# Kernel optimization log

Measured on AMD Instinct MI355X. Metric: run time of the kernel, lower is better.

## Reference

```python
import jax, jax.numpy as jnp
import numpy as np

K = 16  # number of neighbors (self excluded), matches init k
NUM_CLASSES = 100


def setup_inputs() -> dict:
    key = jax.random.key(0)
    kx, ky = jax.random.split(key)
    N, D = 8192, 256
    x = jax.random.normal(kx, (N, D), dtype=jnp.float32)
    y = jax.random.randint(ky, (N,), 0, NUM_CLASSES, dtype=jnp.int64)
    return {"x": x, "y": y}


def _knn_loss(x, y):
    N = x.shape[0]
    k = min(K, N - 1)
    # Pairwise squared Euclidean distances via Gram trick: [N, N]
    sq_norms = jnp.sum(x * x, axis=1)
    sq = sq_norms[:, None] + sq_norms[None, :] - 2.0 * (x @ x.T)
    sq = jnp.maximum(sq, 0.0)
    eye = jnp.eye(N, dtype=bool)
    # Keep sqrt grad-safe on the (excluded) diagonal by placing a dummy 1.0 there.
    d = jnp.sqrt(jnp.where(eye, 1.0, sq))  # [N, N] Euclidean distances

    # k nearest neighbors excluding self (BallTree query k+1 then drop col 0).
    d_for_knn = jnp.where(eye, jnp.inf, d)
    _, nn_idx = jax.lax.top_k(-d_for_knn, k)  # [N, k] indices of smallest distances

    # distances = exp(-d); denominator sums over all j != i.
    exp_d = jnp.where(eye, 0.0, jnp.exp(-d))
    denom = jnp.sum(exp_d, axis=1)  # [N]

    # log(exp(-d_in) / denom_i) = -d_in - log(denom_i)
    nn_d = jnp.take_along_axis(d, nn_idx, axis=1)          # [N, k]
    log_p = -nn_d - jnp.log(denom)[:, None]                 # [N, k]

    # Only neighbors with matching label contribute; rows with none are skipped.
    match = (y[nn_idx] == y[:, None]).astype(x.dtype)       # [N, k]
    cnt = jnp.sum(match, axis=1)                            # [N]
    row_mean = jnp.where(cnt > 0, jnp.sum(log_p * match, axis=1) / jnp.maximum(cnt, 1.0), 0.0)
    return -jnp.sum(row_mean) / N


def reference(x, y):
    return _knn_loss(x, y)
```

## Files before the change

kernel.cpp:

```cpp
#include <hip/hip_runtime.h>
#include <hip/hip_fp16.h>


typedef __attribute__((ext_vector_type(8))) short s8v;
typedef __attribute__((ext_vector_type(4))) float f32x4;

#define NROW 8192
#define NK   256
#define SAMPN 512
#define TAUR  6
#define PSLOT 2

template <bool B> struct BoolC { static constexpr bool value = B; };

#define OFF_DNP  0
#define OFF_NRM  262144
#define OFF_TAU  294912
#define OFF_XB   327680
#define OFF_SAMP 4521984
#define OFF_PASS 4521984
#define PASS_BYTES (NROW * 512 * 4)

__device__ __forceinline__ unsigned short f2bf(float f) {
  unsigned u = __float_as_uint(f);
  return (unsigned short)((u + 0x7FFFu + ((u >> 16) & 1u)) >> 16);
}

__device__ __forceinline__ void gld16(const void* g, void* l) {
  __builtin_amdgcn_global_load_lds(
      (const __attribute__((address_space(1))) unsigned int*)g,
      (__attribute__((address_space(3))) unsigned int*)l, 16, 0, 0);
}

__device__ __forceinline__ unsigned umin32(unsigned a, unsigned b) { return a < b ? a : b; }

__global__ __launch_bounds__(256) void k_prep(const float* __restrict__ x,
                                              unsigned short* __restrict__ xb,
                                              float* __restrict__ nrm) {
  const int w = threadIdx.x >> 6, l = threadIdx.x & 63;
  const int r = blockIdx.x * 4 + w;
  const float4 xv = *reinterpret_cast<const float4*>(x + r * NK + l * 4);
  float ns = xv.x * xv.x + xv.y * xv.y + xv.z * xv.z + xv.w * xv.w;
  ns += __shfl_xor(ns, 1);  ns += __shfl_xor(ns, 2);  ns += __shfl_xor(ns, 4);
  ns += __shfl_xor(ns, 8);  ns += __shfl_xor(ns, 16); ns += __shfl_xor(ns, 32);
  if (l == 0) nrm[r] = ns;
  ushort4 bv;
  bv.x = f2bf(xv.x); bv.y = f2bf(xv.y); bv.z = f2bf(xv.z); bv.w = f2bf(xv.w);
  const int gs = (l >> 1) ^ (r & 7);
  *reinterpret_cast<ushort4*>(xb + r * NK + gs * 8 + (l & 1) * 4) = bv;
}

__global__ __launch_bounds__(512) void k_samp(const unsigned short* __restrict__ xb,
                                              const float* __restrict__ nrm,
                                              unsigned short* __restrict__ samp) {
  __shared__ __align__(16) unsigned short Bl[64 * NK];
  __shared__ float ncs[64];
  const int tid = threadIdx.x;
  const int w = tid >> 6, l = tid & 63, l15 = l & 15, l4 = l >> 4;
  const int rb = blockIdx.x >> 3, ss = blockIdx.x & 7;
  const int rowbase = rb * 128 + (w >> 1) * 32;
  const int wcol = (w & 1) * 32;

  #pragma unroll
  for (int jj = 0; jj < 4; ++jj) {
    const int unit = jj * 512 + tid;
    const int sc = unit >> 5, gsl = unit & 31;
    const int s = ss * 64 + sc;
    const int jrow = s * 16 + (s & 7);
    gld16(xb + jrow * NK + gsl * 8, &Bl[unit * 8]);
  }
  if (tid < 64) {
    const int s = ss * 64 + tid;
    ncs[tid] = nrm[s * 16 + (s & 7)];
  }

  s8v A[2][8];
  #pragma unroll
  for (int rf = 0; rf < 2; ++rf) {
    const int rr = rowbase + rf * 16 + l15;
    #pragma unroll
    for (int kf = 0; kf < 8; ++kf) {
      const int g = ((kf << 2) | l4) ^ (rr & 7);
      A[rf][kf] = *reinterpret_cast<const s8v*>(xb + rr * NK + g * 8);
    }
  }
  float nr[2][4];
  #pragma unroll
  for (int rf = 0; rf < 2; ++rf)
    #pragma unroll
    for (int q = 0; q < 4; ++q) nr[rf][q] = nrm[rowbase + rf * 16 + l4 * 4 + q];

  __syncthreads();
  f32x4 acc[2][2];
  #pragma unroll
  for (int rf = 0; rf < 2; ++rf) {
    f32x4 z = {0.f, 0.f, 0.f, 0.f};
    acc[rf][0] = z; acc[rf][1] = z;
  }
  #pragma unroll
  for (int kf = 0; kf < 8; ++kf) {
    const int gs = ((kf << 2) | l4) ^ (l15 & 7);
    const s8v b0 = *reinterpret_cast<const s8v*>(&Bl[(wcol + l15) * NK + gs * 8]);
    const s8v b1 = *reinterpret_cast<const s8v*>(&Bl[(wcol + 16 + l15) * NK + gs * 8]);
    #pragma unroll
    for (int rf = 0; rf < 2; ++rf) {
      acc[rf][0] = __builtin_amdgcn_mfma_f32_16x16x32_bf16(A[rf][kf], b0, acc[rf][0], 0, 0, 0);
      acc[rf][1] = __builtin_amdgcn_mfma_f32_16x16x32_bf16(A[rf][kf], b1, acc[rf][1], 0, 0, 0);
    }
  }
  #pragma unroll
  for (int rf = 0; rf < 2; ++rf)
    #pragma unroll
    for (int cf = 0; cf < 2; ++cf) {
      const int scol = ss * 64 + wcol + cf * 16 + l15;
      const int jcol = scol * 16 + (scol & 7);
      const float nc = ncs[wcol + cf * 16 + l15];
      #pragma unroll
      for (int q = 0; q < 4; ++q) {
        const int rowg = rowbase + rf * 16 + l4 * 4 + q;
        const float sq = fmaxf(fmaf(acc[rf][cf][q], -2.0f, nr[rf][q] + nc), 0.0f);
        const float dd = __builtin_amdgcn_sqrtf(sq);
        unsigned short d16 = __half_as_ushort(__float2half(dd));
        if (jcol == rowg) d16 = 0xFFFFu;
        samp[rowg * SAMPN + scol] = d16;
      }
    }
}

__global__ __launch_bounds__(256) void k_tau(const unsigned short* __restrict__ samp,
                                             unsigned* __restrict__ tauk) {
  const int w = threadIdx.x >> 6, l = threadIdx.x & 63;
  const int r = blockIdx.x * 4 + w;
  const uint4 pa = *reinterpret_cast<const uint4*>(samp + r * SAMPN + l * 8);
  unsigned v[8];
  v[0] = pa.x & 0xFFFFu; v[1] = pa.x >> 16; v[2] = pa.y & 0xFFFFu; v[3] = pa.y >> 16;
  v[4] = pa.z & 0xFFFFu; v[5] = pa.z >> 16; v[6] = pa.w & 0xFFFFu; v[7] = pa.w >> 16;
  unsigned m = 0;
  for (int pp = 0; pp < TAUR; ++pp) {
    unsigned lm = v[0];
    #pragma unroll
    for (int j = 1; j < 8; ++j) lm = umin32(lm, v[j]);
    m = lm;
    m = umin32(m, __shfl_xor(m, 1));  m = umin32(m, __shfl_xor(m, 2));
    m = umin32(m, __shfl_xor(m, 4));  m = umin32(m, __shfl_xor(m, 8));
    m = umin32(m, __shfl_xor(m, 16)); m = umin32(m, __shfl_xor(m, 32));
    const unsigned long long bal = __ballot(lm == m);
    const int owner = (int)__ffsll(bal) - 1;
    if (l == owner) {
      bool f = false;
      #pragma unroll
      for (int j = 0; j < 8; ++j)
        if (!f && v[j] == m) { v[j] = 0xFFFFFFFFu; f = true; }
    }
  }
  if (l == 0) tauk[r] = m;
}

__global__ __launch_bounds__(512) void k_main(const unsigned short* __restrict__ xb,
                                              const float* __restrict__ nrm,
                                              const unsigned* __restrict__ tauk,
                                              float* __restrict__ dnp,
                                              unsigned* __restrict__ pass) {
  __shared__ __align__(16) unsigned short Bl[2][64 * NK];
  __shared__ float ncsAll[1024];
  __shared__ float dpart[128];
  const int tid = threadIdx.x;
  const int w = tid >> 6, l = tid & 63, l15 = l & 15, l4 = l >> 4;
  const int rb = blockIdx.x >> 3, cs = blockIdx.x & 7;
  const int rowbase = rb * 128 + (w >> 1) * 32;
  const int wcol = (w & 1) * 32;
  const int colslice = cs * 1024;
  const unsigned long long ltm = (1ull << l) - 1ull;
  const unsigned long long sub = 0xFFFFull << (l4 * 16);

  if (tid < 128) dpart[tid] = 0.0f;
  ncsAll[tid]       = nrm[colslice + tid];
  ncsAll[tid + 512] = nrm[colslice + 512 + tid];

  s8v A[2][8];
  #pragma unroll
  for (int rf = 0; rf < 2; ++rf) {
    const int rr = rowbase + rf * 16 + l15;
    #pragma unroll
    for (int kf = 0; kf < 8; ++kf) {
      const int g = ((kf << 2) | l4) ^ (rr & 7);
      A[rf][kf] = *reinterpret_cast<const s8v*>(xb + rr * NK + g * 8);
    }
  }
  float nr[2][4], tk2[2][4], dn[2][4];
  #pragma unroll
  for (int rf = 0; rf < 2; ++rf)
    #pragma unroll
    for (int q = 0; q < 4; ++q) {
      const int rowg = rowbase + rf * 16 + l4 * 4 + q;
      nr[rf][q] = nrm[rowg];
      const float tw = __half2float(__ushort_as_half((unsigned short)(tauk[rowg] + 1u)));
      tk2[rf][q] = tw * tw;
      dn[rf][q] = 0.0f;
    }

  auto stage = [&](int buf, int t) {
    const unsigned short* src = xb + (colslice + t * 64) * NK;
    #pragma unroll
    for (int jj = 0; jj < 4; ++jj)
      gld16(src + (jj * 512 + tid) * 8, &Bl[buf][(jj * 512 + w * 64) * 8]);
  };

  const int tdiag = rb * 2 - cs * 16;

  stage(0, 0);
  __syncthreads();

  for (int t = 0; t < 16; ++t) {
    const int cur = t & 1;
    if (t < 15) {
      stage(cur ^ 1, t + 1);
      asm volatile("s_waitcnt vmcnt(4)" ::: "memory");
    }
    __builtin_amdgcn_s_barrier();
    __builtin_amdgcn_sched_barrier(0);
    const int cbase = colslice + t * 64;
    f32x4 acc[2][2];
    #pragma unroll
    for (int rf = 0; rf < 2; ++rf) {
      f32x4 z = {0.f, 0.f, 0.f, 0.f};
      acc[rf][0] = z; acc[rf][1] = z;
    }
    #pragma unroll
    for (int kf = 0; kf < 8; ++kf) {
      const int gs = ((kf << 2) | l4) ^ (l15 & 7);
      const s8v b0 = *reinterpret_cast<const s8v*>(&Bl[cur][(wcol + l15) * NK + gs * 8]);
      const s8v b1 = *reinterpret_cast<const s8v*>(&Bl[cur][(wcol + 16 + l15) * NK + gs * 8]);
      #pragma unroll
      for (int rf = 0; rf < 2; ++rf) {
        acc[rf][0] = __builtin_amdgcn_mfma_f32_16x16x32_bf16(A[rf][kf], b0, acc[rf][0], 0, 0, 0);
        acc[rf][1] = __builtin_amdgcn_mfma_f32_16x16x32_bf16(A[rf][kf], b1, acc[rf][1], 0, 0, 0);
      }
    }
    const float nc0 = ncsAll[t * 64 + wcol + l15];
    const float nc1 = ncsAll[t * 64 + wcol + 16 + l15];
    const int colg0 = cbase + wcol + l15;
    const int colg1 = colg0 + 16;
    const int gt4 = (cs * 16 + t) * 4;
    auto epi = [&](auto dgc) {
      constexpr bool DG = decltype(dgc)::value;
      #pragma unroll
      for (int rf = 0; rf < 2; ++rf)
        #pragma unroll
        for (int q = 0; q < 4; ++q) {
          const int rowg = rowbase + rf * 16 + l4 * 4 + q;
          float sq0 = fmaf(acc[rf][0][q], -2.0f, nr[rf][q] + nc0);
          float sq1 = fmaf(acc[rf][1][q], -2.0f, nr[rf][q] + nc1);
          if (DG) { sq0 = fmaxf(sq0, 0.0f); sq1 = fmaxf(sq1, 0.0f); }
          const float d0 = __builtin_amdgcn_sqrtf(sq0);
          const float d1 = __builtin_amdgcn_sqrtf(sq1);
          float e0 = __expf(-d0), e1 = __expf(-d1);
          bool p0 = sq0 < tk2[rf][q];
          bool p1 = sq1 < tk2[rf][q];
          if (DG) {
            const bool nd0 = (rowg != colg0), nd1 = (rowg != colg1);
            e0 = nd0 ? e0 : 0.0f;  e1 = nd1 ? e1 : 0.0f;
            p0 = p0 && nd0;  p1 = p1 && nd1;
          }
          dn[rf][q] += e0 + e1;
          const unsigned long long m0 = __ballot(p0);
          const unsigned long long m1 = __ballot(p1);
          if ((m0 | m1) != 0ull) {
            const int r0 = __popcll(m0 & sub & ltm);
            const int r1 = __popcll(m1 & sub & ltm);
            if (p0 && r0 < PSLOT) {
              const unsigned d16 = __half_as_ushort(__float2half(d0));
              pass[rowg * 512 + gt4 + r0] = (d16 << 16) | (unsigned)colg0;
            }
            if (p1 && r1 < PSLOT) {
              const unsigned d16 = __half_as_ushort(__float2half(d1));
              pass[rowg * 512 + gt4 + 2 + r1] = (d16 << 16) | (unsigned)colg1;
            }
          }
        }
    };
    if (t == tdiag || t == tdiag + 1) epi(BoolC<true>{});
    else                              epi(BoolC<false>{});
    __builtin_amdgcn_s_barrier();
  }
  #pragma unroll
  for (int rf = 0; rf < 2; ++rf)
    #pragma unroll
    for (int q = 0; q < 4; ++q) {
      float vs = dn[rf][q];
      vs += __shfl_xor(vs, 1); vs += __shfl_xor(vs, 2);
      vs += __shfl_xor(vs, 4); vs += __shfl_xor(vs, 8);
      if (l15 == 0) atomicAdd(&dpart[(w >> 1) * 32 + rf * 16 + l4 * 4 + q], vs);
    }
  __syncthreads();
  if (tid < 128) dnp[(rb * 128 + tid) * 8 + cs] = dpart[tid];
}

__global__ __launch_bounds__(256) void k_fin(const unsigned* __restrict__ pass,
                                             const float* __restrict__ dnp,
                                             const int* __restrict__ y,
                                             float* __restrict__ out) {
  const int w = threadIdx.x >> 6, l = threadIdx.x & 63;
  const int r = blockIdx.x * 4 + w;
  unsigned kk[8];
  const uint4 pa = *reinterpret_cast<const uint4*>(pass + r * 512 + l * 8);
  const uint4 pb = *reinterpret_cast<const uint4*>(pass + r * 512 + l * 8 + 4);
  kk[0] = pa.x; kk[1] = pa.y; kk[2] = pa.z; kk[3] = pa.w;
  kk[4] = pb.x; kk[5] = pb.y; kk[6] = pb.z; kk[7] = pb.w;
  unsigned myKey = 0xFFFFFFFFu;
  for (int pp = 0; pp < 16; ++pp) {
    unsigned lm = kk[0];
    #pragma unroll
    for (int j = 1; j < 8; ++j) lm = umin32(lm, kk[j]);
    unsigned m = lm;
    m = umin32(m, __shfl_xor(m, 1));  m = umin32(m, __shfl_xor(m, 2));
    m = umin32(m, __shfl_xor(m, 4));  m = umin32(m, __shfl_xor(m, 8));
    m = umin32(m, __shfl_xor(m, 16)); m = umin32(m, __shfl_xor(m, 32));
    const unsigned long long bal = __ballot(lm == m);
    const int owner = (int)__ffsll(bal) - 1;
    if (l == owner) {
      bool f = false;
      #pragma unroll
      for (int j = 0; j < 8; ++j)
        if (!f && kk[j] == m) { kk[j] = 0xFFFFFFFFu; f = true; }
    }
    if (l == pp) myKey = m;
  }
  float den = 0.0f;
  #pragma unroll
  for (int cs = 0; cs < 8; ++cs) den += dnp[r * 8 + cs];
  const float logden = __logf(den);
  float contrib = 0.0f, cmf = 0.0f;
  if (l < 16 && myKey != 0xFFFFFFFFu) {
    const int col = (int)(myKey & 0x1FFFu);
    const float dd = __half2float(__ushort_as_half((unsigned short)(myKey >> 16)));
    if (y[col] == y[r]) { contrib = -dd - logden; cmf = 1.0f; }
  }
  contrib += __shfl_xor(contrib, 1);  contrib += __shfl_xor(contrib, 2);
  contrib += __shfl_xor(contrib, 4);  contrib += __shfl_xor(contrib, 8);
  contrib += __shfl_xor(contrib, 16); contrib += __shfl_xor(contrib, 32);
  cmf += __shfl_xor(cmf, 1);  cmf += __shfl_xor(cmf, 2);
  cmf += __shfl_xor(cmf, 4);  cmf += __shfl_xor(cmf, 8);
  cmf += __shfl_xor(cmf, 16); cmf += __shfl_xor(cmf, 32);
  if (l == 0 && cmf > 0.0f)
    atomicAdd(out, (contrib / cmf) * (-1.0f / 8192.0f));
}

extern "C" void kernel_launch(void* const* d_in, const int* in_sizes, int n_in,
                              void* d_out, int out_size, void* d_ws, size_t ws_size,
                              hipStream_t stream) {
  const float* x = (const float*)d_in[0];
  const int* y = (const int*)d_in[1];
  float* out = (float*)d_out;
  char* ws = (char*)d_ws;

  float*          dnp  = (float*)(ws + OFF_DNP);
  float*          nrm  = (float*)(ws + OFF_NRM);
  unsigned*       tauk = (unsigned*)(ws + OFF_TAU);
  unsigned short* xb   = (unsigned short*)(ws + OFF_XB);
  unsigned short* samp = (unsigned short*)(ws + OFF_SAMP);
  unsigned*       pass = (unsigned*)(ws + OFF_PASS);

  k_prep<<<2048, 256, 0, stream>>>(x, xb, nrm);
  k_samp<<<512,  512, 0, stream>>>(xb, nrm, samp);
  k_tau <<<2048, 256, 0, stream>>>(samp, tauk);
  hipMemsetAsync(pass, 0xFF, PASS_BYTES, stream);
  hipMemsetAsync(d_out, 0, sizeof(float), stream);
  k_main<<<512,  512, 0, stream>>>(xb, nrm, tauk, dnp, pass);
  k_fin <<<2048, 256, 0, stream>>>(pass, dnp, y, out);
}
```

Before: 134.3 us.

## Load B fragments directly from global memory, dropping LDS double-buffer and barriers

Removes the shared-memory double buffer for the column tile. Each wave now reads its B fragments straight from global (L2-cached) memory using precomputed swizzled offsets, so the per-tile block barriers and LDS staging are gone. The diagonal-tile test becomes per wave, and launch bounds request 4 blocks per CU so more waves can hide latency. The cost is more global/L2 traffic, because B tiles are no longer shared across the waves in a block, and likely more load latency exposed inside the MFMA loop.

```diff
diff --git a/kernel.cpp b/kernel.cpp
--- a/kernel.cpp
+++ b/kernel.cpp
@@ -156,12 +156,11 @@
   if (l == 0) tauk[r] = m;
 }
 
-__global__ __launch_bounds__(512) void k_main(const unsigned short* __restrict__ xb,
-                                              const float* __restrict__ nrm,
-                                              const unsigned* __restrict__ tauk,
-                                              float* __restrict__ dnp,
-                                              unsigned* __restrict__ pass) {
-  __shared__ __align__(16) unsigned short Bl[2][64 * NK];
+__global__ __launch_bounds__(512, 4) void k_main(const unsigned short* __restrict__ xb,
+                                                 const float* __restrict__ nrm,
+                                                 const unsigned* __restrict__ tauk,
+                                                 float* __restrict__ dnp,
+                                                 unsigned* __restrict__ pass) {
   __shared__ float ncsAll[1024];
   __shared__ float dpart[128];
   const int tid = threadIdx.x;
@@ -187,6 +186,15 @@
       A[rf][kf] = *reinterpret_cast<const s8v*>(xb + rr * NK + g * 8);
     }
   }
+  int preoff[8];
+  {
+    const int lowpart = ((l4 ^ (l15 & 3)) * 16) + ((wcol + l15) * 512);
+    const int x64 = (l15 & 4) ? 64 : 0;
+    #pragma unroll
+    for (int kf = 0; kf < 8; ++kf) preoff[kf] = ((kf * 64) ^ x64) + lowpart;
+  }
+  const char* xbc = (const char*)xb;
+
   float nr[2][4], tk2[2][4], dn[2][4];
   #pragma unroll
   for (int rf = 0; rf < 2; ++rf)
@@ -199,26 +207,13 @@
       dn[rf][q] = 0.0f;
     }
 
-  auto stage = [&](int buf, int t) {
-    const unsigned short* src = xb + (colslice + t * 64) * NK;
-    #pragma unroll
-    for (int jj = 0; jj < 4; ++jj)
-      gld16(src + (jj * 512 + tid) * 8, &Bl[buf][(jj * 512 + w * 64) * 8]);
-  };
-
-  const int tdiag = rb * 2 - cs * 16;
-
-  stage(0, 0);
+  const int dtb = rowbase - colslice;
+  const int tdw = (dtb >= 0 && dtb < 1024) ? (dtb >> 6) : -1;
+
   __syncthreads();
 
   for (int t = 0; t < 16; ++t) {
-    const int cur = t & 1;
-    if (t < 15) {
-      stage(cur ^ 1, t + 1);
-      asm volatile("s_waitcnt vmcnt(4)" ::: "memory");
-    }
-    __builtin_amdgcn_s_barrier();
-    __builtin_amdgcn_sched_barrier(0);
+    const char* bp0 = xbc + (size_t)(colslice + t * 64) * 512;
     const int cbase = colslice + t * 64;
     f32x4 acc[2][2];
     #pragma unroll
@@ -228,9 +223,8 @@
     }
     #pragma unroll
     for (int kf = 0; kf < 8; ++kf) {
-      const int gs = ((kf << 2) | l4) ^ (l15 & 7);
-      const s8v b0 = *reinterpret_cast<const s8v*>(&Bl[cur][(wcol + l15) * NK + gs * 8]);
-      const s8v b1 = *reinterpret_cast<const s8v*>(&Bl[cur][(wcol + 16 + l15) * NK + gs * 8]);
+      const s8v b0 = *reinterpret_cast<const s8v*>(bp0 + preoff[kf]);
+      const s8v b1 = *reinterpret_cast<const s8v*>(bp0 + 8192 + preoff[kf]);
       #pragma unroll
       for (int rf = 0; rf < 2; ++rf) {
         acc[rf][0] = __builtin_amdgcn_mfma_f32_16x16x32_bf16(A[rf][kf], b0, acc[rf][0], 0, 0, 0);
@@ -279,9 +273,8 @@
           }
         }
     };
-    if (t == tdiag || t == tdiag + 1) epi(BoolC<true>{});
-    else                              epi(BoolC<false>{});
-    __builtin_amdgcn_s_barrier();
+    if (t == tdw) epi(BoolC<true>{});
+    else          epi(BoolC<false>{});
   }
   #pragma unroll
   for (int rf = 0; rf < 2; ++rf)
```

New measurement: 168.8 us. 25.7% more time.

## Replace threshold-sampled candidate pass with per-lane running top-2 selection

Applied to the files above, without the earlier changes.

Removes the sampling GEMM kernel, the per-row threshold kernel and the large memset of the pass buffer. In their place, each lane of the main distance kernel keeps a running top-2 of packed (half distance, column) keys in registers and writes them to a compact candidate buffer for the final selection. This cuts two kernel launches, a full-buffer memset and the ballot/popcount compaction in the epilogue. In exchange it adds min/max work per element and more live registers under a tighter launch bound that may cause spills. The simplified sync (syncthreads instead of vmcnt-tuned barriers) may also reduce load overlap, and the top-2-per-lane candidate set can miss true neighbours when three fall in one lane's columns.

```diff
diff --git a/kernel.cpp b/kernel.cpp
--- a/kernel.cpp
+++ b/kernel.cpp
@@ -7,19 +7,13 @@
 
 #define NROW 8192
 #define NK   256
-#define SAMPN 512
-#define TAUR  6
-#define PSLOT 2
 
 template <bool B> struct BoolC { static constexpr bool value = B; };
 
 #define OFF_DNP  0
 #define OFF_NRM  262144
-#define OFF_TAU  294912
-#define OFF_XB   327680
-#define OFF_SAMP 4521984
-#define OFF_PASS 4521984
-#define PASS_BYTES (NROW * 512 * 4)
+#define OFF_XB   294912
+#define OFF_CAND (294912 + 4194304)
 
 __device__ __forceinline__ unsigned short f2bf(float f) {
   unsigned u = __float_as_uint(f);
@@ -33,6 +27,7 @@
 }
 
 __device__ __forceinline__ unsigned umin32(unsigned a, unsigned b) { return a < b ? a : b; }
+__device__ __forceinline__ unsigned umax32(unsigned a, unsigned b) { return a > b ? a : b; }
 
 __global__ __launch_bounds__(256) void k_prep(const float* __restrict__ x,
                                               unsigned short* __restrict__ xb,
@@ -50,117 +45,10 @@
   *reinterpret_cast<ushort4*>(xb + r * NK + gs * 8 + (l & 1) * 4) = bv;
 }
 
-__global__ __launch_bounds__(512) void k_samp(const unsigned short* __restrict__ xb,
-                                              const float* __restrict__ nrm,
-                                              unsigned short* __restrict__ samp) {
-  __shared__ __align__(16) unsigned short Bl[64 * NK];
-  __shared__ float ncs[64];
-  const int tid = threadIdx.x;
-  const int w = tid >> 6, l = tid & 63, l15 = l & 15, l4 = l >> 4;
-  const int rb = blockIdx.x >> 3, ss = blockIdx.x & 7;
-  const int rowbase = rb * 128 + (w >> 1) * 32;
-  const int wcol = (w & 1) * 32;
-
-  #pragma unroll
-  for (int jj = 0; jj < 4; ++jj) {
-    const int unit = jj * 512 + tid;
-    const int sc = unit >> 5, gsl = unit & 31;
-    const int s = ss * 64 + sc;
-    const int jrow = s * 16 + (s & 7);
-    gld16(xb + jrow * NK + gsl * 8, &Bl[unit * 8]);
-  }
-  if (tid < 64) {
-    const int s = ss * 64 + tid;
-    ncs[tid] = nrm[s * 16 + (s & 7)];
-  }
-
-  s8v A[2][8];
-  #pragma unroll
-  for (int rf = 0; rf < 2; ++rf) {
-    const int rr = rowbase + rf * 16 + l15;
-    #pragma unroll
-    for (int kf = 0; kf < 8; ++kf) {
-      const int g = ((kf << 2) | l4) ^ (rr & 7);
-      A[rf][kf] = *reinterpret_cast<const s8v*>(xb + rr * NK + g * 8);
-    }
-  }
-  float nr[2][4];
-  #pragma unroll
-  for (int rf = 0; rf < 2; ++rf)
-    #pragma unroll
-    for (int q = 0; q < 4; ++q) nr[rf][q] = nrm[rowbase + rf * 16 + l4 * 4 + q];
-
-  __syncthreads();
-  f32x4 acc[2][2];
-  #pragma unroll
-  for (int rf = 0; rf < 2; ++rf) {
-    f32x4 z = {0.f, 0.f, 0.f, 0.f};
-    acc[rf][0] = z; acc[rf][1] = z;
-  }
-  #pragma unroll
-  for (int kf = 0; kf < 8; ++kf) {
-    const int gs = ((kf << 2) | l4) ^ (l15 & 7);
-    const s8v b0 = *reinterpret_cast<const s8v*>(&Bl[(wcol + l15) * NK + gs * 8]);
-    const s8v b1 = *reinterpret_cast<const s8v*>(&Bl[(wcol + 16 + l15) * NK + gs * 8]);
-    #pragma unroll
-    for (int rf = 0; rf < 2; ++rf) {
-      acc[rf][0] = __builtin_amdgcn_mfma_f32_16x16x32_bf16(A[rf][kf], b0, acc[rf][0], 0, 0, 0);
-      acc[rf][1] = __builtin_amdgcn_mfma_f32_16x16x32_bf16(A[rf][kf], b1, acc[rf][1], 0, 0, 0);
-    }
-  }
-  #pragma unroll
-  for (int rf = 0; rf < 2; ++rf)
-    #pragma unroll
-    for (int cf = 0; cf < 2; ++cf) {
-      const int scol = ss * 64 + wcol + cf * 16 + l15;
-      const int jcol = scol * 16 + (scol & 7);
-      const float nc = ncs[wcol + cf * 16 + l15];
-      #pragma unroll
-      for (int q = 0; q < 4; ++q) {
-        const int rowg = rowbase + rf * 16 + l4 * 4 + q;
-        const float sq = fmaxf(fmaf(acc[rf][cf][q], -2.0f, nr[rf][q] + nc), 0.0f);
-        const float dd = __builtin_amdgcn_sqrtf(sq);
-        unsigned short d16 = __half_as_ushort(__float2half(dd));
-        if (jcol == rowg) d16 = 0xFFFFu;
-        samp[rowg * SAMPN + scol] = d16;
-      }
-    }
-}
-
-__global__ __launch_bounds__(256) void k_tau(const unsigned short* __restrict__ samp,
-                                             unsigned* __restrict__ tauk) {
-  const int w = threadIdx.x >> 6, l = threadIdx.x & 63;
-  const int r = blockIdx.x * 4 + w;
-  const uint4 pa = *reinterpret_cast<const uint4*>(samp + r * SAMPN + l * 8);
-  unsigned v[8];
-  v[0] = pa.x & 0xFFFFu; v[1] = pa.x >> 16; v[2] = pa.y & 0xFFFFu; v[3] = pa.y >> 16;
-  v[4] = pa.z & 0xFFFFu; v[5] = pa.z >> 16; v[6] = pa.w & 0xFFFFu; v[7] = pa.w >> 16;
-  unsigned m = 0;
-  for (int pp = 0; pp < TAUR; ++pp) {
-    unsigned lm = v[0];
-    #pragma unroll
-    for (int j = 1; j < 8; ++j) lm = umin32(lm, v[j]);
-    m = lm;
-    m = umin32(m, __shfl_xor(m, 1));  m = umin32(m, __shfl_xor(m, 2));
-    m = umin32(m, __shfl_xor(m, 4));  m = umin32(m, __shfl_xor(m, 8));
-    m = umin32(m, __shfl_xor(m, 16)); m = umin32(m, __shfl_xor(m, 32));
-    const unsigned long long bal = __ballot(lm == m);
-    const int owner = (int)__ffsll(bal) - 1;
-    if (l == owner) {
-      bool f = false;
-      #pragma unroll
-      for (int j = 0; j < 8; ++j)
-        if (!f && v[j] == m) { v[j] = 0xFFFFFFFFu; f = true; }
-    }
-  }
-  if (l == 0) tauk[r] = m;
-}
-
-__global__ __launch_bounds__(512) void k_main(const unsigned short* __restrict__ xb,
-                                              const float* __restrict__ nrm,
-                                              const unsigned* __restrict__ tauk,
-                                              float* __restrict__ dnp,
-                                              unsigned* __restrict__ pass) {
+__global__ __launch_bounds__(512, 4) void k_main(const unsigned short* __restrict__ xb,
+                                                 const float* __restrict__ nrm,
+                                                 float* __restrict__ dnp,
+                                                 unsigned* __restrict__ cand) {
   __shared__ __align__(16) unsigned short Bl[2][64 * NK];
   __shared__ float ncsAll[1024];
   __shared__ float dpart[128];
@@ -170,8 +58,6 @@
   const int rowbase = rb * 128 + (w >> 1) * 32;
   const int wcol = (w & 1) * 32;
   const int colslice = cs * 1024;
-  const unsigned long long ltm = (1ull << l) - 1ull;
-  const unsigned long long sub = 0xFFFFull << (l4 * 16);
 
   if (tid < 128) dpart[tid] = 0.0f;
   ncsAll[tid]       = nrm[colslice + tid];
@@ -187,16 +73,16 @@
       A[rf][kf] = *reinterpret_cast<const s8v*>(xb + rr * NK + g * 8);
     }
   }
-  float nr[2][4], tk2[2][4], dn[2][4];
+  float nr[2][4], dn[2][4];
+  unsigned s0[2][4], s1[2][4];
   #pragma unroll
   for (int rf = 0; rf < 2; ++rf)
     #pragma unroll
     for (int q = 0; q < 4; ++q) {
-      const int rowg = rowbase + rf * 16 + l4 * 4 + q;
-      nr[rf][q] = nrm[rowg];
-      const float tw = __half2float(__ushort_as_half((unsigned short)(tauk[rowg] + 1u)));
-      tk2[rf][q] = tw * tw;
+      nr[rf][q] = nrm[rowbase + rf * 16 + l4 * 4 + q];
       dn[rf][q] = 0.0f;
+      s0[rf][q] = 0xFFFFFFFFu;
+      s1[rf][q] = 0xFFFFFFFFu;
     }
 
   auto stage = [&](int buf, int t) {
@@ -206,19 +92,14 @@
       gld16(src + (jj * 512 + tid) * 8, &Bl[buf][(jj * 512 + w * 64) * 8]);
   };
 
-  const int tdiag = rb * 2 - cs * 16;
+  const int dtb = rowbase - colslice;
+  const int tdw = (dtb >= 0 && dtb < 1024) ? (dtb >> 6) : -1;
 
   stage(0, 0);
-  __syncthreads();
-
   for (int t = 0; t < 16; ++t) {
     const int cur = t & 1;
-    if (t < 15) {
-      stage(cur ^ 1, t + 1);
-      asm volatile("s_waitcnt vmcnt(4)" ::: "memory");
-    }
-    __builtin_amdgcn_s_barrier();
-    __builtin_amdgcn_sched_barrier(0);
+    __syncthreads();
+    if (t + 1 < 16) stage(cur ^ 1, t + 1);
     const int cbase = colslice + t * 64;
     f32x4 acc[2][2];
     #pragma unroll
@@ -239,50 +120,48 @@
     }
     const float nc0 = ncsAll[t * 64 + wcol + l15];
     const float nc1 = ncsAll[t * 64 + wcol + 16 + l15];
-    const int colg0 = cbase + wcol + l15;
-    const int colg1 = colg0 + 16;
-    const int gt4 = (cs * 16 + t) * 4;
+    const unsigned colg0 = (unsigned)(cbase + wcol + l15);
+    const unsigned colg1 = colg0 + 16;
     auto epi = [&](auto dgc) {
       constexpr bool DG = decltype(dgc)::value;
       #pragma unroll
       for (int rf = 0; rf < 2; ++rf)
         #pragma unroll
         for (int q = 0; q < 4; ++q) {
-          const int rowg = rowbase + rf * 16 + l4 * 4 + q;
+          const unsigned rowg = (unsigned)(rowbase + rf * 16 + l4 * 4 + q);
           float sq0 = fmaf(acc[rf][0][q], -2.0f, nr[rf][q] + nc0);
           float sq1 = fmaf(acc[rf][1][q], -2.0f, nr[rf][q] + nc1);
           if (DG) { sq0 = fmaxf(sq0, 0.0f); sq1 = fmaxf(sq1, 0.0f); }
           const float d0 = __builtin_amdgcn_sqrtf(sq0);
           const float d1 = __builtin_amdgcn_sqrtf(sq1);
           float e0 = __expf(-d0), e1 = __expf(-d1);
-          bool p0 = sq0 < tk2[rf][q];
-          bool p1 = sq1 < tk2[rf][q];
+          unsigned k0 = ((unsigned)__half_as_ushort(__float2half(d0)) << 16) | colg0;
+          unsigned k1 = ((unsigned)__half_as_ushort(__float2half(d1)) << 16) | colg1;
           if (DG) {
             const bool nd0 = (rowg != colg0), nd1 = (rowg != colg1);
-            e0 = nd0 ? e0 : 0.0f;  e1 = nd1 ? e1 : 0.0f;
-            p0 = p0 && nd0;  p1 = p1 && nd1;
+            e0 = nd0 ? e0 : 0.0f;          e1 = nd1 ? e1 : 0.0f;
+            k0 = nd0 ? k0 : 0xFFFFFFFFu;   k1 = nd1 ? k1 : 0xFFFFFFFFu;
           }
           dn[rf][q] += e0 + e1;
-          const unsigned long long m0 = __ballot(p0);
-          const unsigned long long m1 = __ballot(p1);
-          if ((m0 | m1) != 0ull) {
-            const int r0 = __popcll(m0 & sub & ltm);
-            const int r1 = __popcll(m1 & sub & ltm);
-            if (p0 && r0 < PSLOT) {
-              const unsigned d16 = __half_as_ushort(__float2half(d0));
-              pass[rowg * 512 + gt4 + r0] = (d16 << 16) | (unsigned)colg0;
-            }
-            if (p1 && r1 < PSLOT) {
-              const unsigned d16 = __half_as_ushort(__float2half(d1));
-              pass[rowg * 512 + gt4 + 2 + r1] = (d16 << 16) | (unsigned)colg1;
-            }
-          }
+          unsigned ev = umax32(s0[rf][q], k0);
+          s0[rf][q] = umin32(s0[rf][q], k0);
+          s1[rf][q] = umin32(s1[rf][q], ev);
+          ev = umax32(s0[rf][q], k1);
+          s0[rf][q] = umin32(s0[rf][q], k1);
+          s1[rf][q] = umin32(s1[rf][q], ev);
         }
     };
-    if (t == tdiag || t == tdiag + 1) epi(BoolC<true>{});
-    else                              epi(BoolC<false>{});
-    __builtin_amdgcn_s_barrier();
-  }
+    if (t == tdw) epi(BoolC<true>{});
+    else          epi(BoolC<false>{});
+  }
+  #pragma unroll
+  for (int rf = 0; rf < 2; ++rf)
+    #pragma unroll
+    for (int q = 0; q < 4; ++q) {
+      const int rowg = rowbase + rf * 16 + l4 * 4 + q;
+      uint2 pr; pr.x = s0[rf][q]; pr.y = s1[rf][q];
+      *reinterpret_cast<uint2*>(&cand[rowg * 512 + cs * 64 + (w & 1) * 32 + l15 * 2]) = pr;
+    }
   #pragma unroll
   for (int rf = 0; rf < 2; ++rf)
     #pragma unroll
@@ -296,15 +175,15 @@
   if (tid < 128) dnp[(rb * 128 + tid) * 8 + cs] = dpart[tid];
 }
 
-__global__ __launch_bounds__(256) void k_fin(const unsigned* __restrict__ pass,
+__global__ __launch_bounds__(256) void k_fin(const unsigned* __restrict__ cand,
                                              const float* __restrict__ dnp,
                                              const int* __restrict__ y,
                                              float* __restrict__ out) {
   const int w = threadIdx.x >> 6, l = threadIdx.x & 63;
   const int r = blockIdx.x * 4 + w;
   unsigned kk[8];
-  const uint4 pa = *reinterpret_cast<const uint4*>(pass + r * 512 + l * 8);
-  const uint4 pb = *reinterpret_cast<const uint4*>(pass + r * 512 + l * 8 + 4);
+  const uint4 pa = *reinterpret_cast<const uint4*>(cand + r * 512 + l * 8);
+  const uint4 pb = *reinterpret_cast<const uint4*>(cand + r * 512 + l * 8 + 4);
   kk[0] = pa.x; kk[1] = pa.y; kk[2] = pa.z; kk[3] = pa.w;
   kk[4] = pb.x; kk[5] = pb.y; kk[6] = pb.z; kk[7] = pb.w;
   unsigned myKey = 0xFFFFFFFFu;
@@ -356,16 +235,11 @@
 
   float*          dnp  = (float*)(ws + OFF_DNP);
   float*          nrm  = (float*)(ws + OFF_NRM);
-  unsigned*       tauk = (unsigned*)(ws + OFF_TAU);
   unsigned short* xb   = (unsigned short*)(ws + OFF_XB);
-  unsigned short* samp = (unsigned short*)(ws + OFF_SAMP);
-  unsigned*       pass = (unsigned*)(ws + OFF_PASS);
-
+  unsigned*       cand = (unsigned*)(ws + OFF_CAND);
+
+  hipMemsetAsync(d_out, 0, sizeof(float), stream);
   k_prep<<<2048, 256, 0, stream>>>(x, xb, nrm);
-  k_samp<<<512,  512, 0, stream>>>(xb, nrm, samp);
-  k_tau <<<2048, 256, 0, stream>>>(samp, tauk);
-  hipMemsetAsync(pass, 0xFF, PASS_BYTES, stream);
-  hipMemsetAsync(d_out, 0, sizeof(float), stream);
-  k_main<<<512,  512, 0, stream>>>(xb, nrm, tauk, dnp, pass);
-  k_fin <<<2048, 256, 0, stream>>>(pass, dnp, y, out);
-}
+  k_main<<<512,  512, 0, stream>>>(xb, nrm, dnp, cand);
+  k_fin <<<2048, 256, 0, stream>>>(cand, dnp, y, out);
+}
```

Measured after the change: 118.6 us. 11.7% less time.
